# Performance work log

Hardware: AMD Instinct MI355X
Metric: run time of the kernel (lower is better)

The kernel has to match this reference:

```python
import jax, jax.numpy as jnp
import numpy as np
from jax.scipy.special import logsumexp

N_ALPHA = 8192
N_BETA = 8192
N_LAYERS = 16


def setup_inputs() -> dict:
    key = jax.random.key(0)
    k1, k2, k3 = jax.random.split(key, 3)
    alpha = jax.random.uniform(k1, (N_ALPHA,), jnp.float32, 1e-3, 1.0)
    alpha = alpha / alpha.sum()
    beta = jax.random.uniform(k2, (N_BETA,), jnp.float32, 1e-3, 1.0)
    beta = beta / beta.sum()
    C = jax.random.uniform(k3, (N_ALPHA, N_BETA), jnp.float32, 0.0, 1.0)
    eps = jnp.float32(0.1)
    return {"alpha": alpha, "beta": beta, "C": C, "eps": eps}


def reference(alpha, beta, C, eps):
    # Log-domain Sinkhorn iterations (tol=None -> run all n_layers).
    log_alpha = jnp.log(alpha)
    log_beta = jnp.log(beta)

    def step(carry, _):
        _, g = carry
        # log_dot_exp(C, g, eps): logsumexp over n_beta axis of (-C + g[None,:]) / eps
        f = eps * (log_alpha - logsumexp((g[None, :] - C) / eps, axis=-1))
        # log_dot_exp(C.T, f, eps): logsumexp over n_alpha axis of (-C + f[:,None]) / eps
        g_new = eps * (log_beta - logsumexp((f[:, None] - C) / eps, axis=0))
        return (f, g_new), None

    init = (jnp.zeros_like(alpha), jnp.zeros_like(beta))
    (f, g), _ = jax.lax.scan(step, init, None, length=N_LAYERS)
    return f, g
```

## Files before the change

kernel.cpp:

```cpp
#include <hip/hip_runtime.h>

#define NA 8192
#define NB 8192
#define N_LAYERS 16
#define ROWS_PER_VC 64
#define N_VC (NA / ROWS_PER_VC)

typedef _Float16 half_t;
typedef _Float16 half8_t __attribute__((ext_vector_type(8)));
typedef float float4_t __attribute__((ext_vector_type(4)));

template <bool WRITE_E>
__global__ __launch_bounds__(256) void sink_u_first(
    const float* __restrict__ C, const float* __restrict__ alpha,
    const float* __restrict__ d_eps, half_t* __restrict__ E,
    float* __restrict__ u)
{
    const int row = blockIdx.x;
    const int t = threadIdx.x;
    const float inv_eps = 1.0f / d_eps[0];
    const float4_t* Crow = (const float4_t*)(C + (size_t)row * NB);
    half8_t* Erow = (half8_t*)(E + (size_t)row * NB);

    float s = 0.0f;
#pragma unroll
    for (int k = 0; k < 4; ++k) {
        const int g = k * 256 + t;
        float4_t c0 = Crow[2 * g];
        float4_t c1 = Crow[2 * g + 1];
        float e0 = __expf(-c0.x * inv_eps);
        float e1 = __expf(-c0.y * inv_eps);
        float e2 = __expf(-c0.z * inv_eps);
        float e3 = __expf(-c0.w * inv_eps);
        float e4 = __expf(-c1.x * inv_eps);
        float e5 = __expf(-c1.y * inv_eps);
        float e6 = __expf(-c1.z * inv_eps);
        float e7 = __expf(-c1.w * inv_eps);
        if (WRITE_E) {
            half8_t h;
            h[0] = (_Float16)e0; h[1] = (_Float16)e1;
            h[2] = (_Float16)e2; h[3] = (_Float16)e3;
            h[4] = (_Float16)e4; h[5] = (_Float16)e5;
            h[6] = (_Float16)e6; h[7] = (_Float16)e7;
            Erow[g] = h;
        }
        s += ((e0 + e1) + (e2 + e3)) + ((e4 + e5) + (e6 + e7));
    }

    __shared__ float sm[256];
    sm[t] = s;
    __syncthreads();
    for (int off = 128; off > 0; off >>= 1) {
        if (t < off) sm[t] += sm[t + off];
        __syncthreads();
    }
    if (t == 0) u[row] = alpha[row] / sm[0];
}

template <bool USE_E>
__global__ __launch_bounds__(256) void sink_u_step(
    const void* __restrict__ mat, const float* __restrict__ v,
    const float* __restrict__ alpha, const float* __restrict__ d_eps,
    float* __restrict__ u)
{
    const int row = blockIdx.x;
    const int t = threadIdx.x;
    const float4_t* vv = (const float4_t*)v;
    float s = 0.0f;

    if (USE_E) {
        const half8_t* Erow = (const half8_t*)mat + (size_t)row * (NB / 8);
#pragma unroll
        for (int k = 0; k < 4; ++k) {
            const int g = k * 256 + t;
            half8_t e = Erow[g];
            float4_t w0 = vv[2 * g], w1 = vv[2 * g + 1];
            s += (float)e[0] * w0.x + (float)e[1] * w0.y +
                 (float)e[2] * w0.z + (float)e[3] * w0.w;
            s += (float)e[4] * w1.x + (float)e[5] * w1.y +
                 (float)e[6] * w1.z + (float)e[7] * w1.w;
        }
    } else {
        const float inv_eps = 1.0f / d_eps[0];
        const float4_t* Crow = (const float4_t*)mat + (size_t)row * (NB / 4);
#pragma unroll
        for (int k = 0; k < 8; ++k) {
            const int g = k * 256 + t;
            float4_t c = Crow[g];
            float4_t w = vv[g];
            s += __expf(-c.x * inv_eps) * w.x + __expf(-c.y * inv_eps) * w.y +
                 __expf(-c.z * inv_eps) * w.z + __expf(-c.w * inv_eps) * w.w;
        }
    }

    __shared__ float sm[256];
    sm[t] = s;
    __syncthreads();
    for (int off = 128; off > 0; off >>= 1) {
        if (t < off) sm[t] += sm[t + off];
        __syncthreads();
    }
    if (t == 0) u[row] = alpha[row] / sm[0];
}

template <bool USE_E>
__global__ __launch_bounds__(256) void sink_v_partial(
    const void* __restrict__ mat, const float* __restrict__ u,
    const float* __restrict__ d_eps, float* __restrict__ partial)
{
    const int cc = blockIdx.x;
    const int rc = blockIdx.y;
    const int t = threadIdx.x;
    const int row0 = rc * ROWS_PER_VC;

    float acc[8];
#pragma unroll
    for (int k = 0; k < 8; ++k) acc[k] = 0.0f;

    if (USE_E) {
        const half8_t* Eb = (const half8_t*)mat;
        const int g = cc * 256 + t;
#pragma unroll 8
        for (int r = 0; r < ROWS_PER_VC; ++r) {
            const float ur = u[row0 + r];
            half8_t e = Eb[(size_t)(row0 + r) * (NB / 8) + g];
#pragma unroll
            for (int k = 0; k < 8; ++k) acc[k] += ur * (float)e[k];
        }
    } else {
        const float inv_eps = 1.0f / d_eps[0];
        const float4_t* Cb = (const float4_t*)mat;
        const int g = (cc * 256 + t) * 2;
#pragma unroll 4
        for (int r = 0; r < ROWS_PER_VC; ++r) {
            const float ur = u[row0 + r];
            float4_t c0 = Cb[(size_t)(row0 + r) * (NB / 4) + g];
            float4_t c1 = Cb[(size_t)(row0 + r) * (NB / 4) + g + 1];
            acc[0] += ur * __expf(-c0.x * inv_eps);
            acc[1] += ur * __expf(-c0.y * inv_eps);
            acc[2] += ur * __expf(-c0.z * inv_eps);
            acc[3] += ur * __expf(-c0.w * inv_eps);
            acc[4] += ur * __expf(-c1.x * inv_eps);
            acc[5] += ur * __expf(-c1.y * inv_eps);
            acc[6] += ur * __expf(-c1.z * inv_eps);
            acc[7] += ur * __expf(-c1.w * inv_eps);
        }
    }

    float4_t o0 = {acc[0], acc[1], acc[2], acc[3]};
    float4_t o1 = {acc[4], acc[5], acc[6], acc[7]};
    float4_t* p = (float4_t*)(partial + (size_t)rc * NB + (size_t)(cc * 256 + t) * 8);
    p[0] = o0;
    p[1] = o1;
}

__global__ __launch_bounds__(256) void sink_v_combine(
    const float* __restrict__ partial, const float* __restrict__ beta,
    float* __restrict__ v)
{
    const int col = blockIdx.x * 256 + threadIdx.x;
    float s = 0.0f;
#pragma unroll 8
    for (int rc = 0; rc < N_VC; ++rc) s += partial[(size_t)rc * NB + col];
    v[col] = beta[col] / s;
}

__global__ __launch_bounds__(256) void sink_finalize(
    const float* __restrict__ u, const float* __restrict__ v,
    const float* __restrict__ d_eps, float* __restrict__ out)
{
    const int i = blockIdx.x * 256 + threadIdx.x;
    const float eps = d_eps[0];
    if (i < NA) {
        out[i] = eps * logf(u[i]);
    } else if (i < NA + NB) {
        out[i] = eps * logf(v[i - NA]);
    }
}

extern "C" void kernel_launch(void* const* d_in, const int* in_sizes, int n_in,
                              void* d_out, int out_size, void* d_ws, size_t ws_size,
                              hipStream_t stream)
{
    const float* alpha = (const float*)d_in[0];
    const float* beta  = (const float*)d_in[1];
    const float* C     = (const float*)d_in[2];
    const float* d_eps = (const float*)d_in[3];
    float* out = (float*)d_out;

    const size_t eBytes = (size_t)NA * NB * sizeof(half_t);
    const size_t pBytes = (size_t)N_VC * NB * sizeof(float);
    const size_t vecBytes = (size_t)NA * sizeof(float);

    char* ws = (char*)d_ws;
    const bool useE = ws_size >= eBytes + pBytes + 2 * vecBytes;

    size_t off = 0;
    half_t* E = nullptr;
    if (useE) { E = (half_t*)ws; off += eBytes; }
    float* partial = (float*)(ws + off); off += pBytes;
    float* u = (float*)(ws + off); off += vecBytes;
    float* v = (float*)(ws + off); off += vecBytes;

    const dim3 blk(256);
    const dim3 gridRow(NA);
    const dim3 gridVP(NB / 2048, N_VC);
    const dim3 gridVC(NB / 256);

    for (int layer = 0; layer < N_LAYERS; ++layer) {
        if (layer == 0) {
            if (useE)
                sink_u_first<true><<<gridRow, blk, 0, stream>>>(C, alpha, d_eps, E, u);
            else
                sink_u_first<false><<<gridRow, blk, 0, stream>>>(C, alpha, d_eps, nullptr, u);
        } else {
            if (useE)
                sink_u_step<true><<<gridRow, blk, 0, stream>>>(E, v, alpha, d_eps, u);
            else
                sink_u_step<false><<<gridRow, blk, 0, stream>>>(C, v, alpha, d_eps, u);
        }
        if (useE)
            sink_v_partial<true><<<gridVP, blk, 0, stream>>>(E, u, d_eps, partial);
        else
            sink_v_partial<false><<<gridVP, blk, 0, stream>>>(C, u, d_eps, partial);
        sink_v_combine<<<gridVC, blk, 0, stream>>>(partial, beta, v);
    }
    sink_finalize<<<dim3((NA + NB) / 256), blk, 0, stream>>>(u, v, d_eps, out);
}
```

Before: 1.168 ms.

## Fuse row-normalization and column partial sums into one pass over E

Merges the u-step and v-partial kernels into a single kernel. Each block owns a contiguous chunk of rows, computes each row's u via a wave-shuffle reduction, and immediately accumulates u-weighted column partials. This halves the per-iteration reads of the fp16 E matrix. Rows are double-buffered in registers to prefetch the next pair, and the combine kernel is reorganized to reduce more partials (up to 512 row chunks) with a shared-memory split. In exchange it adds per-row-pair barriers and a larger partial buffer to reduce.

Result: faster. 1.111 ms (-5.0%).

```diff
diff --git a/kernel.cpp b/kernel.cpp
--- a/kernel.cpp
+++ b/kernel.cpp
@@ -3,166 +3,204 @@
 #define NA 8192
 #define NB 8192
 #define N_LAYERS 16
-#define ROWS_PER_VC 64
-#define N_VC (NA / ROWS_PER_VC)
 
 typedef _Float16 half_t;
 typedef _Float16 half8_t __attribute__((ext_vector_type(8)));
 typedef float float4_t __attribute__((ext_vector_type(4)));
 
-template <bool WRITE_E>
-__global__ __launch_bounds__(256) void sink_u_first(
-    const float* __restrict__ C, const float* __restrict__ alpha,
-    const float* __restrict__ d_eps, half_t* __restrict__ E,
-    float* __restrict__ u)
-{
-    const int row = blockIdx.x;
+__device__ __forceinline__ void barrier_lds() {
+    asm volatile("s_waitcnt lgkmcnt(0)" ::: "memory");
+    __builtin_amdgcn_s_barrier();
+    asm volatile("" ::: "memory");
+}
+
+template <bool READ_C, bool WRITE_E, bool HAS_V>
+__global__ __launch_bounds__(256, 2) void sink_fused(
+    const float* __restrict__ C, const half_t* __restrict__ Ein,
+    half_t* __restrict__ Eout, const float* __restrict__ v,
+    const float* __restrict__ alpha, const float* __restrict__ d_eps,
+    float* __restrict__ u, float* __restrict__ partial, int n_groups)
+{
     const int t = threadIdx.x;
-    const float inv_eps = 1.0f / d_eps[0];
-    const float4_t* Crow = (const float4_t*)(C + (size_t)row * NB);
-    half8_t* Erow = (half8_t*)(E + (size_t)row * NB);
-
-    float s = 0.0f;
-#pragma unroll
-    for (int k = 0; k < 4; ++k) {
-        const int g = k * 256 + t;
-        float4_t c0 = Crow[2 * g];
-        float4_t c1 = Crow[2 * g + 1];
-        float e0 = __expf(-c0.x * inv_eps);
-        float e1 = __expf(-c0.y * inv_eps);
-        float e2 = __expf(-c0.z * inv_eps);
-        float e3 = __expf(-c0.w * inv_eps);
-        float e4 = __expf(-c1.x * inv_eps);
-        float e5 = __expf(-c1.y * inv_eps);
-        float e6 = __expf(-c1.z * inv_eps);
-        float e7 = __expf(-c1.w * inv_eps);
-        if (WRITE_E) {
-            half8_t h;
-            h[0] = (_Float16)e0; h[1] = (_Float16)e1;
-            h[2] = (_Float16)e2; h[3] = (_Float16)e3;
-            h[4] = (_Float16)e4; h[5] = (_Float16)e5;
-            h[6] = (_Float16)e6; h[7] = (_Float16)e7;
-            Erow[g] = h;
-        }
-        s += ((e0 + e1) + (e2 + e3)) + ((e4 + e5) + (e6 + e7));
-    }
-
-    __shared__ float sm[256];
-    sm[t] = s;
-    __syncthreads();
-    for (int off = 128; off > 0; off >>= 1) {
-        if (t < off) sm[t] += sm[t + off];
-        __syncthreads();
-    }
-    if (t == 0) u[row] = alpha[row] / sm[0];
-}
-
-template <bool USE_E>
-__global__ __launch_bounds__(256) void sink_u_step(
-    const void* __restrict__ mat, const float* __restrict__ v,
-    const float* __restrict__ alpha, const float* __restrict__ d_eps,
-    float* __restrict__ u)
-{
-    const int row = blockIdx.x;
-    const int t = threadIdx.x;
-    const float4_t* vv = (const float4_t*)v;
-    float s = 0.0f;
-
-    if (USE_E) {
-        const half8_t* Erow = (const half8_t*)mat + (size_t)row * (NB / 8);
+    const int rc = blockIdx.x;
+    const int row0 = rc * (n_groups * 2);
+    __shared__ float sred[2][8];
+
+    float4_t w0[4], w1[4];
+    if constexpr (HAS_V) {
+        const float4_t* vv = (const float4_t*)v;
 #pragma unroll
         for (int k = 0; k < 4; ++k) {
             const int g = k * 256 + t;
-            half8_t e = Erow[g];
-            float4_t w0 = vv[2 * g], w1 = vv[2 * g + 1];
-            s += (float)e[0] * w0.x + (float)e[1] * w0.y +
-                 (float)e[2] * w0.z + (float)e[3] * w0.w;
-            s += (float)e[4] * w1.x + (float)e[5] * w1.y +
-                 (float)e[6] * w1.z + (float)e[7] * w1.w;
+            w0[k] = vv[2 * g];
+            w1[k] = vv[2 * g + 1];
+        }
+    }
+
+    float acc[4][8];
+#pragma unroll
+    for (int k = 0; k < 4; ++k)
+#pragma unroll
+        for (int j = 0; j < 8; ++j) acc[k][j] = 0.0f;
+
+    auto usum = [&](float rs0, float rs1, int par) -> float2 {
+#pragma unroll
+        for (int m = 1; m < 64; m <<= 1) {
+            rs0 += __shfl_xor(rs0, m, 64);
+            rs1 += __shfl_xor(rs1, m, 64);
+        }
+        const int lane = t & 63, wid = t >> 6;
+        if (lane == 0) { sred[par][wid * 2] = rs0; sred[par][wid * 2 + 1] = rs1; }
+        barrier_lds();
+        const float S0 = (sred[par][0] + sred[par][2]) + (sred[par][4] + sred[par][6]);
+        const float S1 = (sred[par][1] + sred[par][3]) + (sred[par][5] + sred[par][7]);
+        return make_float2(S0, S1);
+    };
+
+    if constexpr (!READ_C) {
+        const half8_t* Eb = (const half8_t*)Ein;
+        half8_t bufA[2][4], bufB[2][4];
+
+        auto load = [&](half8_t (&d)[2][4], int r0) {
+#pragma unroll
+            for (int rr = 0; rr < 2; ++rr)
+#pragma unroll
+                for (int k = 0; k < 4; ++k)
+                    d[rr][k] = Eb[(size_t)(r0 + rr) * (NB / 8) + k * 256 + t];
+        };
+
+        auto step = [&](half8_t (&cur)[2][4], half8_t (&nxt)[2][4], int r0,
+                        int par, bool pf) {
+            if (pf) load(nxt, r0 + 2);
+            const float a0 = alpha[r0], a1 = alpha[r0 + 1];
+            float rs0 = 0.0f, rs1 = 0.0f;
+#pragma unroll
+            for (int k = 0; k < 4; ++k) {
+                rs0 += (float)cur[0][k][0] * w0[k].x + (float)cur[0][k][1] * w0[k].y +
+                       (float)cur[0][k][2] * w0[k].z + (float)cur[0][k][3] * w0[k].w +
+                       (float)cur[0][k][4] * w1[k].x + (float)cur[0][k][5] * w1[k].y +
+                       (float)cur[0][k][6] * w1[k].z + (float)cur[0][k][7] * w1[k].w;
+                rs1 += (float)cur[1][k][0] * w0[k].x + (float)cur[1][k][1] * w0[k].y +
+                       (float)cur[1][k][2] * w0[k].z + (float)cur[1][k][3] * w0[k].w +
+                       (float)cur[1][k][4] * w1[k].x + (float)cur[1][k][5] * w1[k].y +
+                       (float)cur[1][k][6] * w1[k].z + (float)cur[1][k][7] * w1[k].w;
+            }
+            const float2 S = usum(rs0, rs1, par);
+            const float u0 = a0 / S.x, u1 = a1 / S.y;
+            if (t == 0) { u[r0] = u0; u[r0 + 1] = u1; }
+#pragma unroll
+            for (int k = 0; k < 4; ++k)
+#pragma unroll
+                for (int j = 0; j < 8; ++j)
+                    acc[k][j] += u0 * (float)cur[0][k][j] + u1 * (float)cur[1][k][j];
+        };
+
+        load(bufA, row0);
+        for (int s = 0; s < n_groups; s += 2) {
+            step(bufA, bufB, row0 + 2 * s, 0, true);
+            step(bufB, bufA, row0 + 2 * (s + 1), 1, s + 2 < n_groups);
         }
     } else {
         const float inv_eps = 1.0f / d_eps[0];
-        const float4_t* Crow = (const float4_t*)mat + (size_t)row * (NB / 4);
-#pragma unroll
-        for (int k = 0; k < 8; ++k) {
-            const int g = k * 256 + t;
-            float4_t c = Crow[g];
-            float4_t w = vv[g];
-            s += __expf(-c.x * inv_eps) * w.x + __expf(-c.y * inv_eps) * w.y +
-                 __expf(-c.z * inv_eps) * w.z + __expf(-c.w * inv_eps) * w.w;
-        }
-    }
-
-    __shared__ float sm[256];
-    sm[t] = s;
-    __syncthreads();
-    for (int off = 128; off > 0; off >>= 1) {
-        if (t < off) sm[t] += sm[t + off];
-        __syncthreads();
-    }
-    if (t == 0) u[row] = alpha[row] / sm[0];
-}
-
-template <bool USE_E>
-__global__ __launch_bounds__(256) void sink_v_partial(
-    const void* __restrict__ mat, const float* __restrict__ u,
-    const float* __restrict__ d_eps, float* __restrict__ partial)
-{
-    const int cc = blockIdx.x;
-    const int rc = blockIdx.y;
-    const int t = threadIdx.x;
-    const int row0 = rc * ROWS_PER_VC;
-
-    float acc[8];
-#pragma unroll
-    for (int k = 0; k < 8; ++k) acc[k] = 0.0f;
-
-    if (USE_E) {
-        const half8_t* Eb = (const half8_t*)mat;
-        const int g = cc * 256 + t;
-#pragma unroll 8
-        for (int r = 0; r < ROWS_PER_VC; ++r) {
-            const float ur = u[row0 + r];
-            half8_t e = Eb[(size_t)(row0 + r) * (NB / 8) + g];
-#pragma unroll
-            for (int k = 0; k < 8; ++k) acc[k] += ur * (float)e[k];
-        }
-    } else {
-        const float inv_eps = 1.0f / d_eps[0];
-        const float4_t* Cb = (const float4_t*)mat;
-        const int g = (cc * 256 + t) * 2;
-#pragma unroll 4
-        for (int r = 0; r < ROWS_PER_VC; ++r) {
-            const float ur = u[row0 + r];
-            float4_t c0 = Cb[(size_t)(row0 + r) * (NB / 4) + g];
-            float4_t c1 = Cb[(size_t)(row0 + r) * (NB / 4) + g + 1];
-            acc[0] += ur * __expf(-c0.x * inv_eps);
-            acc[1] += ur * __expf(-c0.y * inv_eps);
-            acc[2] += ur * __expf(-c0.z * inv_eps);
-            acc[3] += ur * __expf(-c0.w * inv_eps);
-            acc[4] += ur * __expf(-c1.x * inv_eps);
-            acc[5] += ur * __expf(-c1.y * inv_eps);
-            acc[6] += ur * __expf(-c1.z * inv_eps);
-            acc[7] += ur * __expf(-c1.w * inv_eps);
-        }
-    }
-
-    float4_t o0 = {acc[0], acc[1], acc[2], acc[3]};
-    float4_t o1 = {acc[4], acc[5], acc[6], acc[7]};
-    float4_t* p = (float4_t*)(partial + (size_t)rc * NB + (size_t)(cc * 256 + t) * 8);
-    p[0] = o0;
-    p[1] = o1;
+        const float4_t* Cb = (const float4_t*)C;
+        float4_t bufA[2][8], bufB[2][8];
+
+        auto load = [&](float4_t (&d)[2][8], int r0) {
+#pragma unroll
+            for (int rr = 0; rr < 2; ++rr)
+#pragma unroll
+                for (int k = 0; k < 4; ++k) {
+                    const int g = k * 256 + t;
+                    d[rr][2 * k]     = Cb[(size_t)(r0 + rr) * (NB / 4) + 2 * g];
+                    d[rr][2 * k + 1] = Cb[(size_t)(r0 + rr) * (NB / 4) + 2 * g + 1];
+                }
+        };
+
+        auto step = [&](float4_t (&cur)[2][8], float4_t (&nxt)[2][8], int r0,
+                        int par, bool pf) {
+            if (pf) load(nxt, r0 + 2);
+            const float a0 = alpha[r0], a1 = alpha[r0 + 1];
+            half8_t h[2][4];
+            float rs0 = 0.0f, rs1 = 0.0f;
+#pragma unroll
+            for (int rr = 0; rr < 2; ++rr) {
+                float rs = 0.0f;
+#pragma unroll
+                for (int k = 0; k < 4; ++k) {
+                    const float4_t c0 = cur[rr][2 * k], c1 = cur[rr][2 * k + 1];
+                    const float e0 = __expf(-c0.x * inv_eps);
+                    const float e1 = __expf(-c0.y * inv_eps);
+                    const float e2 = __expf(-c0.z * inv_eps);
+                    const float e3 = __expf(-c0.w * inv_eps);
+                    const float e4 = __expf(-c1.x * inv_eps);
+                    const float e5 = __expf(-c1.y * inv_eps);
+                    const float e6 = __expf(-c1.z * inv_eps);
+                    const float e7 = __expf(-c1.w * inv_eps);
+                    h[rr][k][0] = (_Float16)e0; h[rr][k][1] = (_Float16)e1;
+                    h[rr][k][2] = (_Float16)e2; h[rr][k][3] = (_Float16)e3;
+                    h[rr][k][4] = (_Float16)e4; h[rr][k][5] = (_Float16)e5;
+                    h[rr][k][6] = (_Float16)e6; h[rr][k][7] = (_Float16)e7;
+                    if constexpr (HAS_V) {
+                        rs += e0 * w0[k].x + e1 * w0[k].y + e2 * w0[k].z + e3 * w0[k].w +
+                              e4 * w1[k].x + e5 * w1[k].y + e6 * w1[k].z + e7 * w1[k].w;
+                    } else {
+                        rs += ((e0 + e1) + (e2 + e3)) + ((e4 + e5) + (e6 + e7));
+                    }
+                }
+                if (rr == 0) rs0 = rs; else rs1 = rs;
+            }
+            if constexpr (WRITE_E) {
+#pragma unroll
+                for (int rr = 0; rr < 2; ++rr)
+#pragma unroll
+                    for (int k = 0; k < 4; ++k)
+                        ((half8_t*)Eout)[(size_t)(r0 + rr) * (NB / 8) + k * 256 + t] = h[rr][k];
+            }
+            const float2 S = usum(rs0, rs1, par);
+            const float u0 = a0 / S.x, u1 = a1 / S.y;
+            if (t == 0) { u[r0] = u0; u[r0 + 1] = u1; }
+#pragma unroll
+            for (int k = 0; k < 4; ++k)
+#pragma unroll
+                for (int j = 0; j < 8; ++j)
+                    acc[k][j] += u0 * (float)h[0][k][j] + u1 * (float)h[1][k][j];
+        };
+
+        load(bufA, row0);
+        for (int s = 0; s < n_groups; s += 2) {
+            step(bufA, bufB, row0 + 2 * s, 0, true);
+            step(bufB, bufA, row0 + 2 * (s + 1), 1, s + 2 < n_groups);
+        }
+    }
+
+#pragma unroll
+    for (int k = 0; k < 4; ++k) {
+        float4_t o0 = {acc[k][0], acc[k][1], acc[k][2], acc[k][3]};
+        float4_t o1 = {acc[k][4], acc[k][5], acc[k][6], acc[k][7]};
+        float4_t* p = (float4_t*)(partial + (size_t)rc * NB + (size_t)(k * 256 + t) * 8);
+        p[0] = o0;
+        p[1] = o1;
+    }
 }
 
 __global__ __launch_bounds__(256) void sink_v_combine(
     const float* __restrict__ partial, const float* __restrict__ beta,
-    float* __restrict__ v)
-{
-    const int col = blockIdx.x * 256 + threadIdx.x;
+    float* __restrict__ v, int nvc)
+{
+    const int c = blockIdx.x * 32 + (threadIdx.x & 31);
+    const int sl = threadIdx.x >> 5;
     float s = 0.0f;
-#pragma unroll 8
-    for (int rc = 0; rc < N_VC; ++rc) s += partial[(size_t)rc * NB + col];
-    v[col] = beta[col] / s;
+#pragma unroll 4
+    for (int i = sl; i < nvc; i += 8) s += partial[(size_t)i * NB + c];
+    __shared__ float sm[8][32];
+    sm[sl][threadIdx.x & 31] = s;
+    __syncthreads();
+    if (threadIdx.x < 32) {
+        float tot = 0.0f;
+#pragma unroll
+        for (int k = 0; k < 8; ++k) tot += sm[k][threadIdx.x];
+        v[c] = beta[c] / tot;
+    }
 }
 
 __global__ __launch_bounds__(256) void sink_finalize(
@@ -188,42 +226,49 @@
     const float* d_eps = (const float*)d_in[3];
     float* out = (float*)d_out;
 
-    const size_t eBytes = (size_t)NA * NB * sizeof(half_t);
-    const size_t pBytes = (size_t)N_VC * NB * sizeof(float);
+    const size_t eBytes   = (size_t)NA * NB * sizeof(half_t);
     const size_t vecBytes = (size_t)NA * sizeof(float);
 
+    int nvc = 0;
+    bool useE = false;
+    if      (ws_size >= eBytes + (size_t)512 * NB * 4 + 2 * vecBytes) { useE = true; nvc = 512; }
+    else if (ws_size >= eBytes + (size_t)256 * NB * 4 + 2 * vecBytes) { useE = true; nvc = 256; }
+    else if (ws_size >= eBytes + (size_t)128 * NB * 4 + 2 * vecBytes) { useE = true; nvc = 128; }
+    else if (ws_size >= (size_t)512 * NB * 4 + 2 * vecBytes)          { nvc = 512; }
+    else if (ws_size >= (size_t)256 * NB * 4 + 2 * vecBytes)          { nvc = 256; }
+    else                                                              { nvc = 128; }
+
     char* ws = (char*)d_ws;
-    const bool useE = ws_size >= eBytes + pBytes + 2 * vecBytes;
-
     size_t off = 0;
     half_t* E = nullptr;
     if (useE) { E = (half_t*)ws; off += eBytes; }
-    float* partial = (float*)(ws + off); off += pBytes;
+    float* partial = (float*)(ws + off); off += (size_t)nvc * NB * sizeof(float);
     float* u = (float*)(ws + off); off += vecBytes;
-    float* v = (float*)(ws + off); off += vecBytes;
-
+    float* v = (float*)(ws + off);
+
+    const int ng = (NA / nvc) / 2;
     const dim3 blk(256);
-    const dim3 gridRow(NA);
-    const dim3 gridVP(NB / 2048, N_VC);
-    const dim3 gridVC(NB / 256);
+    const dim3 gridF(nvc);
+    const dim3 gridC(NB / 32);
+    const dim3 gridFin((NA + NB) / 256);
 
     for (int layer = 0; layer < N_LAYERS; ++layer) {
         if (layer == 0) {
             if (useE)
-                sink_u_first<true><<<gridRow, blk, 0, stream>>>(C, alpha, d_eps, E, u);
+                sink_fused<true, true, false><<<gridF, blk, 0, stream>>>(
+                    C, nullptr, E, nullptr, alpha, d_eps, u, partial, ng);
             else
-                sink_u_first<false><<<gridRow, blk, 0, stream>>>(C, alpha, d_eps, nullptr, u);
+                sink_fused<true, false, false><<<gridF, blk, 0, stream>>>(
+                    C, nullptr, nullptr, nullptr, alpha, d_eps, u, partial, ng);
         } else {
             if (useE)
-                sink_u_step<true><<<gridRow, blk, 0, stream>>>(E, v, alpha, d_eps, u);
+                sink_fused<false, false, true><<<gridF, blk, 0, stream>>>(
+                    nullptr, E, nullptr, v, alpha, d_eps, u, partial, ng);
             else
-                sink_u_step<false><<<gridRow, blk, 0, stream>>>(C, v, alpha, d_eps, u);
-        }
-        if (useE)
-            sink_v_partial<true><<<gridVP, blk, 0, stream>>>(E, u, d_eps, partial);
-        else
-            sink_v_partial<false><<<gridVP, blk, 0, stream>>>(C, u, d_eps, partial);
-        sink_v_combine<<<gridVC, blk, 0, stream>>>(partial, beta, v);
-    }
-    sink_finalize<<<dim3((NA + NB) / 256), blk, 0, stream>>>(u, v, d_eps, out);
-}
+                sink_fused<true, false, true><<<gridF, blk, 0, stream>>>(
+                    C, nullptr, nullptr, v, alpha, d_eps, u, partial, ng);
+        }
+        sink_v_combine<<<gridC, blk, 0, stream>>>(partial, beta, v, nvc);
+    }
+    sink_finalize<<<gridFin, blk, 0, stream>>>(u, v, d_eps, out);
+}
```
